# Optimization experiments

Measured on AMD Instinct MI355X. Metric: run time of the kernel, lower is better.

## Reference

```python
import jax, jax.numpy as jnp
import numpy as np
import math


def l1_cdist(a, b):
    """L1 pairwise distance sum_d |a_i - b_j| without materializing (..,n,m,d).
    a: (..., n, d), b: (..., m, d) -> (..., n, m). Scans over feature dim."""
    aT = jnp.moveaxis(a, -1, 0)  # (d, ..., n)
    bT = jnp.moveaxis(b, -1, 0)  # (d, ..., m)
    init = jnp.zeros(a.shape[:-1] + (b.shape[-2],), a.dtype)

    def body(acc, ab):
        ai, bi = ab
        return acc + jnp.abs(ai[..., :, None] - bi[..., None, :]), None

    return jax.lax.scan(body, init, (aT, bT))[0]


def sq_l2_cdist(a, b):
    """Squared euclidean pairwise distance via GEMM (matches cdist(p=2)**2, clamped >=0)."""
    a2 = jnp.sum(a * a, axis=-1)
    b2 = jnp.sum(b * b, axis=-1)
    ab = jnp.einsum('...nd,...md->...nm', a, b)
    return jnp.maximum(a2[..., :, None] + b2[..., None, :] - 2.0 * ab, 0.0)


def proxy_delta_linear(x, weight, gain):
    """ProxyDeltaLinearV68 forward. x: (B,T,Din), weight: (Dout,Din), gain: (1,Dout,1)."""
    B, T, Din = x.shape
    Dout = weight.shape[0]
    x_act = jnp.tanh(x).reshape(-1, Din)   # (B*T, Din)
    w_act = jnp.tanh(weight)               # (Dout, Din)
    l1_mean = jax.lax.stop_gradient(l1_cdist(x_act, w_act)) / Din
    l2_sq_mean = sq_l2_cdist(x_act, w_act) / Din
    # (l1 - l2).detach() + l2
    dist = jax.lax.stop_gradient(l1_mean - l2_sq_mean) + l2_sq_mean
    out = (1.0 - dist).reshape(B, T, Dout)
    return (out - 0.5) * gain.reshape(1, 1, Dout)


def attention_forward(x, mask, wq_weight, wq_gain, wk_weight, wk_gain,
                      wv_weight, wv_gain, wo_weight, wo_bias, gamma, rho):
    B, T, C = x.shape
    H = gamma.shape[1]
    d = C // H
    scale = math.sqrt(d)

    q = jnp.tanh(proxy_delta_linear(x, wq_weight, wq_gain))
    k = jnp.tanh(proxy_delta_linear(x, wk_weight, wk_gain))
    v = proxy_delta_linear(x, wv_weight, wv_gain)

    q = q.reshape(B, T, H, d).transpose(0, 2, 1, 3).reshape(B * H, T, d)
    k = k.reshape(B, T, H, d).transpose(0, 2, 1, 3).reshape(B * H, T, d)
    v = v.reshape(B, T, H, d).transpose(0, 2, 1, 3)  # (B,H,T,d)

    l1_mean = jax.lax.stop_gradient(l1_cdist(q, k)) / d       # (B*H,T,T)
    l2_sq_mean = sq_l2_cdist(q, k) / d
    dist_proxy = jax.lax.stop_gradient(l1_mean - l2_sq_mean) + l2_sq_mean
    dist_proxy = dist_proxy.reshape(B, H, T, T)

    dist_scaled = dist_proxy * scale
    dist_final_sq = dist_scaled * dist_scaled
    gamma_pos = jax.nn.softplus(gamma)  # (1,H,1,1)
    rho_pos = jax.nn.softplus(rho)
    base_kernel = 1.0 / (1.0 + gamma_pos * dist_final_sq + 1e-6)
    attn_weights = base_kernel ** rho_pos
    attn_weights = jnp.where(mask == 0, 0.0, attn_weights)
    attn_probs = attn_weights / (jnp.sum(attn_weights, axis=-1, keepdims=True) + 1e-6)

    out = jnp.einsum('bhqk,bhkd->bhqd', attn_probs, v)
    out = out.transpose(0, 2, 1, 3).reshape(B, T, C)
    return out @ wo_weight.T + wo_bias


def setup_inputs() -> dict:
    B, T, C, H = 2, 2048, 512, 8
    key = jax.random.key(0)
    ks = jax.random.split(key, 8)
    x = jax.random.normal(ks[0], (B, T, C), dtype=jnp.float32)
    mask = jnp.tril(jnp.ones((T, T), dtype=jnp.int32))[None, None]  # causal (1,1,T,T)
    mk = lambda k: jax.random.normal(k, (C, C), dtype=jnp.float32) * 0.1
    return {
        'x': x,
        'mask': mask,
        'wq_weight': mk(ks[1]), 'wq_gain': jnp.full((1, C, 1), 2.0, jnp.float32),
        'wk_weight': mk(ks[2]), 'wk_gain': jnp.full((1, C, 1), 2.0, jnp.float32),
        'wv_weight': mk(ks[3]), 'wv_gain': jnp.full((1, C, 1), 2.0, jnp.float32),
        'wo_weight': jax.random.normal(ks[4], (C, C), dtype=jnp.float32) * (1.0 / math.sqrt(C)),
        'wo_bias': jnp.zeros((C,), dtype=jnp.float32),
        'gamma': jnp.ones((1, H, 1, 1), dtype=jnp.float32),
        'rho': jnp.full((1, H, 1, 1), 2.0, jnp.float32),
    }


def reference(x, mask, wq_weight, wq_gain, wk_weight, wk_gain,
              wv_weight, wv_gain, wo_weight, wo_bias, gamma, rho):
    return attention_forward(x, mask, wq_weight, wq_gain, wk_weight, wk_gain,
                             wv_weight, wv_gain, wo_weight, wo_bias, gamma, rho)
```

## Files before the change

### kernel.cpp

```cpp
#include <hip/hip_runtime.h>
#include <hip/hip_bf16.h>

#define T_SEQ 2048
#define CDIM 512
#define HDIM 8
#define DHEAD 64
#define BT 4096

#define PSTR 36
__global__ __launch_bounds__(256, 1) void proj_l1(
    const float* __restrict__ x,
    const float* __restrict__ wq, const float* __restrict__ wk, const float* __restrict__ wv,
    const float* __restrict__ gq,  const float* __restrict__ gk,  const float* __restrict__ gv,
    float* __restrict__ oq, float* __restrict__ okk, float* __restrict__ ov)
{
    __shared__ float As[64][PSTR];
    __shared__ float Bs[128][PSTR];

    const int z = blockIdx.z;
    const float* w    = (z == 0) ? wq : (z == 1) ? wk : wv;
    const float* gain = (z == 0) ? gq : (z == 1) ? gk : gv;
    float* outp       = (z == 0) ? oq : (z == 1) ? okk : ov;

    const int row0 = blockIdx.y * 64;
    const int col0 = blockIdx.x * 128;
    const int tid = threadIdx.x;
    const int tx = tid & 15, ty = tid >> 4;

    float acc[4][8];
    #pragma unroll
    for (int i = 0; i < 4; ++i)
        #pragma unroll
        for (int j = 0; j < 8; ++j) acc[i][j] = 0.f;

    for (int k0 = 0; k0 < CDIM; k0 += 32) {
        __syncthreads();
        #pragma unroll
        for (int q = 0; q < 2; ++q) {
            const int fi = tid + 256 * q;
            const int r = fi >> 3, c4 = 4 * (fi & 7);
            float4 t = *(const float4*)&x[(size_t)(row0 + r) * CDIM + k0 + c4];
            t.x = tanhf(t.x); t.y = tanhf(t.y); t.z = tanhf(t.z); t.w = tanhf(t.w);
            *(float4*)&As[r][c4] = t;
        }
        #pragma unroll
        for (int q = 0; q < 4; ++q) {
            const int fi = tid + 256 * q;
            const int r = fi >> 3, c4 = 4 * (fi & 7);
            float4 t = *(const float4*)&w[(size_t)(col0 + r) * CDIM + k0 + c4];
            t.x = tanhf(t.x); t.y = tanhf(t.y); t.z = tanhf(t.z); t.w = tanhf(t.w);
            *(float4*)&Bs[r][c4] = t;
        }
        __syncthreads();

        #pragma unroll 2
        for (int kk = 0; kk < 32; kk += 4) {
            float4 a4[4];
            #pragma unroll
            for (int i = 0; i < 4; ++i) a4[i] = *(const float4*)&As[ty + 16*i][kk];
            #pragma unroll
            for (int jh = 0; jh < 2; ++jh) {
                float4 b4[4];
                #pragma unroll
                for (int jj = 0; jj < 4; ++jj)
                    b4[jj] = *(const float4*)&Bs[tx + 16*(4*jh + jj)][kk];
                #pragma unroll
                for (int i = 0; i < 4; ++i)
                    #pragma unroll
                    for (int jj = 0; jj < 4; ++jj)
                        acc[i][4*jh + jj] += fabsf(a4[i].x - b4[jj].x) + fabsf(a4[i].y - b4[jj].y)
                                           + fabsf(a4[i].z - b4[jj].z) + fabsf(a4[i].w - b4[jj].w);
            }
        }
    }

    float gcol[8];
    #pragma unroll
    for (int j = 0; j < 8; ++j) gcol[j] = gain[col0 + tx + 16*j];

    #pragma unroll
    for (int i = 0; i < 4; ++i) {
        const int r = row0 + ty + 16*i;
        #pragma unroll
        for (int j = 0; j < 8; ++j) {
            const int c = col0 + tx + 16*j;
            float val = (0.5f - acc[i][j] * (1.0f / 512.0f)) * gcol[j];
            if (z < 2) val = tanhf(val);
            outp[(size_t)r * CDIM + c] = val;
        }
    }
}

__global__ __launch_bounds__(256, 1) void attn_l1(
    const float* __restrict__ qg, const float* __restrict__ kg, const float* __restrict__ vg,
    const float* __restrict__ gamma, const float* __restrict__ rho,
    float* __restrict__ slabv, float* __restrict__ slabs)
{
    __shared__ float Qs[128][68];
    __shared__ float Vs[64][68];
    __shared__ float KW[4608];

    const int bh = blockIdx.x;
    const int b = bh >> 3, h = bh & 7;

    int slot = blockIdx.y;
    int s = 15, c = 0;
    for (;; --s) {
        const int nc = (s >> 2) + 1;
        if (slot < nc) { c = slot; break; }
        slot -= nc;
    }
    const int i0 = s * 128;
    const int kt0 = 8 * c;
    const int kt1 = min(8 * c + 7, 2 * s + 1);

    const int tid = threadIdx.x;
    const int tx = tid & 15, ty = tid >> 4;

    const float gp = log1pf(__expf(gamma[h]));
    const float rp = log1pf(__expf(rho[h]));
    const float gp64 = gp * (1.0f / 64.0f);
    const float mrho = -rp;

    const size_t hb = (size_t)b * T_SEQ * CDIM + h * DHEAD;

    {
        const int gr = tid >> 3;
        const int gc = (tid & 7) * 4;
        #pragma unroll
        for (int p = 0; p < 4; ++p)
            #pragma unroll
            for (int h2 = 0; h2 < 2; ++h2)
                *(float4*)&Qs[gr + 32*p][gc + 32*h2] =
                    *(const float4*)&qg[hb + (size_t)(i0 + gr + 32*p) * CDIM + gc + 32*h2];
    }

    float4 o4[8];
    float accs[8];
    float l1w[8][4];
    #pragma unroll
    for (int i = 0; i < 8; ++i) {
        o4[i] = make_float4(0.f, 0.f, 0.f, 0.f);
        accs[i] = 0.f;
    }

    for (int kt = kt0; kt <= kt1; ++kt) {
        const int j0 = kt * 64;
        __syncthreads();
        #pragma unroll
        for (int q = 0; q < 4; ++q) {
            const int fi = tid + 256 * q;
            const int r = fi >> 4, c4 = 4 * (fi & 15);
            const size_t off = hb + (size_t)(j0 + r) * CDIM + c4;
            *(float4*)&KW[r * 68 + c4] = *(const float4*)&kg[off];
            *(float4*)&Vs[r][c4]       = *(const float4*)&vg[off];
        }
        __syncthreads();

        #pragma unroll
        for (int i = 0; i < 8; ++i)
            #pragma unroll
            for (int j = 0; j < 4; ++j) l1w[i][j] = 0.f;

        #pragma unroll 2
        for (int d0 = 0; d0 < DHEAD; d0 += 4) {
            float4 a4[8];
            #pragma unroll
            for (int i = 0; i < 8; ++i) a4[i] = *(const float4*)&Qs[ty + 16*i][d0];
            #pragma unroll
            for (int j = 0; j < 4; ++j) {
                const float4 kx = *(const float4*)&KW[(tx + 16*j) * 68 + d0];
                #pragma unroll
                for (int i = 0; i < 8; ++i)
                    l1w[i][j] += fabsf(a4[i].x - kx.x) + fabsf(a4[i].y - kx.y)
                               + fabsf(a4[i].z - kx.z) + fabsf(a4[i].w - kx.w);
            }
        }

        const bool diag = (kt >= 2 * s);
        #pragma unroll
        for (int i = 0; i < 8; ++i)
            #pragma unroll
            for (int j = 0; j < 4; ++j) {
                const float l1 = l1w[i][j];
                const float den = fmaf(gp64 * l1, l1, 1.000001f);
                float wgt = __builtin_amdgcn_exp2f(mrho * __builtin_amdgcn_logf(den));
                if (diag && (j0 + tx + 16*j) > (i0 + ty + 16*i)) wgt = 0.f;
                l1w[i][j] = wgt;
                accs[i] += wgt;
            }

        #pragma unroll
        for (int hh = 0; hh < 2; ++hh) {
            __syncthreads();
            #pragma unroll
            for (int i = 0; i < 8; ++i) {
                KW[(ty + 16*i) * 36 + tx]      = l1w[i][2*hh];
                KW[(ty + 16*i) * 36 + tx + 16] = l1w[i][2*hh + 1];
            }
            __syncthreads();

            #pragma unroll 2
            for (int jc = 0; jc < 32; jc += 4) {
                float4 w4[8], v4[4];
                #pragma unroll
                for (int i = 0; i < 8; ++i)
                    w4[i] = *(const float4*)&KW[(ty + 16*i) * 36 + jc];
                #pragma unroll
                for (int jj = 0; jj < 4; ++jj)
                    v4[jj] = *(const float4*)&Vs[32*hh + jc + jj][tx*4];
                #pragma unroll
                for (int i = 0; i < 8; ++i) {
                    o4[i].x += w4[i].x*v4[0].x + w4[i].y*v4[1].x + w4[i].z*v4[2].x + w4[i].w*v4[3].x;
                    o4[i].y += w4[i].x*v4[0].y + w4[i].y*v4[1].y + w4[i].z*v4[2].y + w4[i].w*v4[3].y;
                    o4[i].z += w4[i].x*v4[0].z + w4[i].y*v4[1].z + w4[i].z*v4[2].z + w4[i].w*v4[3].z;
                    o4[i].w += w4[i].x*v4[0].w + w4[i].y*v4[1].w + w4[i].z*v4[2].w + w4[i].w*v4[3].w;
                }
            }
        }
    }

    #pragma unroll
    for (int i = 0; i < 8; ++i) {
        accs[i] += __shfl_xor(accs[i], 1, 64);
        accs[i] += __shfl_xor(accs[i], 2, 64);
        accs[i] += __shfl_xor(accs[i], 4, 64);
        accs[i] += __shfl_xor(accs[i], 8, 64);
    }

    float* sv = slabv + (size_t)c * ((size_t)BT * CDIM);
    float* ss = slabs + (size_t)c * ((size_t)BT * HDIM);
    #pragma unroll
    for (int i = 0; i < 8; ++i) {
        const int qr = i0 + ty + 16*i;
        if (tx == 0)
            ss[(size_t)(b * T_SEQ + qr) * HDIM + h] = accs[i];
        *(float4*)&sv[hb + (size_t)qr * CDIM + tx*4] = o4[i];
    }
}

__global__ __launch_bounds__(256) void normalize_k(
    const float* __restrict__ slabv, const float* __restrict__ slabs,
    float* __restrict__ ab)
{
    int idx = blockIdx.x * 256 + threadIdx.x;
    const int row = idx >> 7;
    const int col = (idx & 127) << 2;
    const int h = col >> 6;
    const int t = row & (T_SEQ - 1);
    const int nch = ((t >> 7) >> 2) + 1;

    const size_t NV = (size_t)BT * CDIM / 4;
    const size_t NS = (size_t)BT * HDIM;
    float4 v = ((const float4*)slabv)[idx];
    float ssum = slabs[(size_t)row * HDIM + h];
    #pragma unroll
    for (int c = 1; c < 4; ++c) {
        if (c < nch) {
            float4 u = ((const float4*)slabv)[c * NV + idx];
            v.x += u.x; v.y += u.y; v.z += u.z; v.w += u.w;
            ssum += slabs[c * NS + (size_t)row * HDIM + h];
        }
    }
    const float inv = 1.0f / (ssum + 1e-6f);
    v.x *= inv; v.y *= inv; v.z *= inv; v.w *= inv;
    ((float4*)ab)[idx] = v;
}

__global__ __launch_bounds__(256, 1) void out_gemm(
    const float* __restrict__ A, const float* __restrict__ wo,
    const float* __restrict__ bias, float* __restrict__ Y)
{
    __shared__ float As[128][PSTR];
    __shared__ float Bs[64][PSTR];

    const int row0 = blockIdx.y * 128;
    const int col0 = blockIdx.x * 64;
    const int tid = threadIdx.x;
    const int tx = tid & 15, ty = tid >> 4;
    const int lr = tid >> 3;
    const int lc = (tid & 7) * 4;

    float acc[8][4];
    #pragma unroll
    for (int i = 0; i < 8; ++i)
        #pragma unroll
        for (int j = 0; j < 4; ++j) acc[i][j] = 0.f;

    for (int k0 = 0; k0 < CDIM; k0 += 32) {
        __syncthreads();
        #pragma unroll
        for (int p = 0; p < 4; ++p)
            *(float4*)&As[lr + 32*p][lc] =
                *(const float4*)&A[(size_t)(row0 + lr + 32*p) * CDIM + k0 + lc];
        *(float4*)&Bs[lr][lc] = *(const float4*)&wo[(size_t)(col0 + lr) * CDIM + k0 + lc];
        *(float4*)&Bs[lr + 32][lc] = *(const float4*)&wo[(size_t)(col0 + lr + 32) * CDIM + k0 + lc];
        __syncthreads();

        #pragma unroll
        for (int kk = 0; kk < 32; kk += 4) {
            float4 a4[8], b4[4];
            #pragma unroll
            for (int i = 0; i < 8; ++i) a4[i] = *(const float4*)&As[ty + 16*i][kk];
            #pragma unroll
            for (int j = 0; j < 4; ++j) b4[j] = *(const float4*)&Bs[tx + 16*j][kk];
            #pragma unroll
            for (int i = 0; i < 8; ++i)
                #pragma unroll
                for (int j = 0; j < 4; ++j)
                    acc[i][j] += a4[i].x * b4[j].x + a4[i].y * b4[j].y
                               + a4[i].z * b4[j].z + a4[i].w * b4[j].w;
        }
    }

    float bcol[4];
    #pragma unroll
    for (int j = 0; j < 4; ++j) bcol[j] = bias[col0 + tx + 16*j];

    #pragma unroll
    for (int i = 0; i < 8; ++i) {
        const int r = row0 + ty + 16*i;
        #pragma unroll
        for (int j = 0; j < 4; ++j) {
            const int c = col0 + tx + 16*j;
            Y[(size_t)r * CDIM + c] = acc[i][j] + bcol[j];
        }
    }
}

extern "C" void kernel_launch(void* const* d_in, const int* in_sizes, int n_in,
                              void* d_out, int out_size, void* d_ws, size_t ws_size,
                              hipStream_t stream)
{
    (void)in_sizes; (void)n_in; (void)out_size; (void)ws_size;
    const float* x     = (const float*)d_in[0];
    const float* wq    = (const float*)d_in[2];
    const float* gq    = (const float*)d_in[3];
    const float* wk    = (const float*)d_in[4];
    const float* gk    = (const float*)d_in[5];
    const float* wv    = (const float*)d_in[6];
    const float* gv    = (const float*)d_in[7];
    const float* wo    = (const float*)d_in[8];
    const float* wob   = (const float*)d_in[9];
    const float* gamma = (const float*)d_in[10];
    const float* rho   = (const float*)d_in[11];
    float* out = (float*)d_out;

    const size_t NV = (size_t)BT * CDIM;
    const size_t NS = (size_t)BT * HDIM;

    float* ws    = (float*)d_ws;
    float* qb    = ws;
    float* kb    = qb + NV;
    float* vb    = kb + NV;
    float* slabv = vb + NV;
    float* slabs = slabv + 4 * NV;
    float* ab    = slabv + 3 * NV;
    ab = slabs + 4 * NS;

    proj_l1<<<dim3(4, 64, 3), 256, 0, stream>>>(x, wq, wk, wv,
                                                gq, gk, gv, qb, kb, vb);
    attn_l1<<<dim3(16, 40), 256, 0, stream>>>(qb, kb, vb, gamma, rho, slabv, slabs);
    normalize_k<<<2048, 256, 0, stream>>>(slabv, slabs, qb);
    out_gemm<<<dim3(8, 32), 256, 0, stream>>>(qb, wo, wob, out);
}
```

Before: 627.3 us.

## Store Q/K/V tiles as bf16 in shared memory and balance key-tile chunks

The attention kernel now converts Q, K and V to bf16 when staging them into shared memory and widens them back to fp32 for the L1 and weighted-sum math. This halves LDS footprint and load bandwidth per tile, at the cost of extra conversion instructions and reduced precision in the distance computation. Key-tile ranges per chunk are also split evenly across chunks instead of fixed blocks of eight, to balance work among blocks of the same query tile. An unused pointer computation is removed.

```diff
diff --git a/kernel.cpp b/kernel.cpp
--- a/kernel.cpp
+++ b/kernel.cpp
@@ -6,6 +6,15 @@
 #define HDIM 8
 #define DHEAD 64
 #define BT 4096
+
+__device__ __forceinline__ unsigned short f2b(float x) {
+    unsigned u = __float_as_uint(x);
+    u += 0x7fff + ((u >> 16) & 1);
+    return (unsigned short)(u >> 16);
+}
+__device__ __forceinline__ float b2f(unsigned short v) {
+    return __uint_as_float((unsigned)v << 16);
+}
 
 #define PSTR 36
 __global__ __launch_bounds__(256, 1) void proj_l1(
@@ -96,9 +105,10 @@
     const float* __restrict__ gamma, const float* __restrict__ rho,
     float* __restrict__ slabv, float* __restrict__ slabs)
 {
-    __shared__ float Qs[128][68];
-    __shared__ float Vs[64][68];
+    __shared__ unsigned short Qs[128][68];
+    __shared__ unsigned short Vs[64][68];
     __shared__ float KW[4608];
+    unsigned short* Ks = (unsigned short*)KW;
 
     const int bh = blockIdx.x;
     const int b = bh >> 3, h = bh & 7;
@@ -111,8 +121,11 @@
         slot -= nc;
     }
     const int i0 = s * 128;
-    const int kt0 = 8 * c;
-    const int kt1 = min(8 * c + 7, 2 * s + 1);
+    const int ntile = 2 * s + 2;
+    const int nch = (s >> 2) + 1;
+    const int base = ntile / nch, rem = ntile % nch;
+    const int kt0 = c * base + min(c, rem);
+    const int kt1 = kt0 + base + (c < rem ? 1 : 0) - 1;
 
     const int tid = threadIdx.x;
     const int tx = tid & 15, ty = tid >> 4;
@@ -124,15 +137,13 @@
 
     const size_t hb = (size_t)b * T_SEQ * CDIM + h * DHEAD;
 
-    {
-        const int gr = tid >> 3;
-        const int gc = (tid & 7) * 4;
-        #pragma unroll
-        for (int p = 0; p < 4; ++p)
-            #pragma unroll
-            for (int h2 = 0; h2 < 2; ++h2)
-                *(float4*)&Qs[gr + 32*p][gc + 32*h2] =
-                    *(const float4*)&qg[hb + (size_t)(i0 + gr + 32*p) * CDIM + gc + 32*h2];
+    #pragma unroll
+    for (int q = 0; q < 8; ++q) {
+        const int fi = tid + 256 * q;
+        const int r = fi >> 4, c4 = 4 * (fi & 15);
+        float4 t = *(const float4*)&qg[hb + (size_t)(i0 + r) * CDIM + c4];
+        ushort4 u = make_ushort4(f2b(t.x), f2b(t.y), f2b(t.z), f2b(t.w));
+        *(ushort4*)&Qs[r][c4] = u;
     }
 
     float4 o4[8];
@@ -152,8 +163,10 @@
             const int fi = tid + 256 * q;
             const int r = fi >> 4, c4 = 4 * (fi & 15);
             const size_t off = hb + (size_t)(j0 + r) * CDIM + c4;
-            *(float4*)&KW[r * 68 + c4] = *(const float4*)&kg[off];
-            *(float4*)&Vs[r][c4]       = *(const float4*)&vg[off];
+            float4 kt4 = *(const float4*)&kg[off];
+            float4 vt4 = *(const float4*)&vg[off];
+            *(ushort4*)&Ks[r * 68 + c4] = make_ushort4(f2b(kt4.x), f2b(kt4.y), f2b(kt4.z), f2b(kt4.w));
+            *(ushort4*)&Vs[r][c4]       = make_ushort4(f2b(vt4.x), f2b(vt4.y), f2b(vt4.z), f2b(vt4.w));
         }
         __syncthreads();
 
@@ -166,14 +179,18 @@
         for (int d0 = 0; d0 < DHEAD; d0 += 4) {
             float4 a4[8];
             #pragma unroll
-            for (int i = 0; i < 8; ++i) a4[i] = *(const float4*)&Qs[ty + 16*i][d0];
+            for (int i = 0; i < 8; ++i) {
+                ushort4 u = *(const ushort4*)&Qs[ty + 16*i][d0];
+                a4[i] = make_float4(b2f(u.x), b2f(u.y), b2f(u.z), b2f(u.w));
+            }
             #pragma unroll
             for (int j = 0; j < 4; ++j) {
-                const float4 kx = *(const float4*)&KW[(tx + 16*j) * 68 + d0];
+                ushort4 uk = *(const ushort4*)&Ks[(tx + 16*j) * 68 + d0];
+                const float k0f = b2f(uk.x), k1f = b2f(uk.y), k2f = b2f(uk.z), k3f = b2f(uk.w);
                 #pragma unroll
                 for (int i = 0; i < 8; ++i)
-                    l1w[i][j] += fabsf(a4[i].x - kx.x) + fabsf(a4[i].y - kx.y)
-                               + fabsf(a4[i].z - kx.z) + fabsf(a4[i].w - kx.w);
+                    l1w[i][j] += fabsf(a4[i].x - k0f) + fabsf(a4[i].y - k1f)
+                               + fabsf(a4[i].z - k2f) + fabsf(a4[i].w - k3f);
             }
         }
 
@@ -207,8 +224,10 @@
                 for (int i = 0; i < 8; ++i)
                     w4[i] = *(const float4*)&KW[(ty + 16*i) * 36 + jc];
                 #pragma unroll
-                for (int jj = 0; jj < 4; ++jj)
-                    v4[jj] = *(const float4*)&Vs[32*hh + jc + jj][tx*4];
+                for (int jj = 0; jj < 4; ++jj) {
+                    ushort4 uv = *(const ushort4*)&Vs[32*hh + jc + jj][tx*4];
+                    v4[jj] = make_float4(b2f(uv.x), b2f(uv.y), b2f(uv.z), b2f(uv.w));
+                }
                 #pragma unroll
                 for (int i = 0; i < 8; ++i) {
                     o4[i].x += w4[i].x*v4[0].x + w4[i].y*v4[1].x + w4[i].z*v4[2].x + w4[i].w*v4[3].x;
@@ -355,8 +374,6 @@
     float* vb    = kb + NV;
     float* slabv = vb + NV;
     float* slabs = slabv + 4 * NV;
-    float* ab    = slabv + 3 * NV;
-    ab = slabs + 4 * NS;
 
     proj_l1<<<dim3(4, 64, 3), 256, 0, stream>>>(x, wq, wk, wv,
                                                 gq, gk, gv, qb, kb, vb);
```

New measurement: 639.7 us. No clear change (+2.0%).
